# Kernel tuning notes

Hardware: AMD Instinct MI355X
Metric: run time of the kernel (lower is better)

## Reference

```python
import jax, jax.numpy as jnp
import numpy as np

NUM_HEADS = 12
NUM_LANDMARKS = 64


def iterative_inv(K, n_iter=6):
    # K: [B, H, L, L]; Newton-Schulz-style pseudo-inverse iteration
    I = jnp.eye(K.shape[-1], dtype=K.dtype)
    denom = jnp.max(jnp.sum(K, axis=-2), axis=-1)[..., None, None]  # [B,H,1,1]
    V = jnp.swapaxes(K, -1, -2) / denom
    for _ in range(n_iter):
        KV = K @ V
        V = 0.25 * V @ (13.0 * I - KV @ (15.0 * I - KV @ (7.0 * I - KV)))
    return V


def setup_inputs() -> dict:
    key = jax.random.key(0)
    k1, k2, k3, k4 = jax.random.split(key, 4)
    B, N, C = 8, 4096, 768
    x = jax.random.normal(k1, (B, N, C), dtype=jnp.float32)
    w_qkv = jax.random.normal(k2, (C, 3 * C), dtype=jnp.float32) * 0.02
    w_proj = jax.random.normal(k3, (C, C), dtype=jnp.float32) * 0.02
    b_proj = jax.random.normal(k4, (C,), dtype=jnp.float32) * 0.02
    return {"x": x, "w_qkv": w_qkv, "w_proj": w_proj, "b_proj": b_proj}


def reference(x, w_qkv, w_proj, b_proj):
    B, N, C = x.shape
    H, L = NUM_HEADS, NUM_LANDMARKS
    D = C // H
    scale = D ** 0.5

    qkv = (x @ w_qkv).reshape(B, N, 3, H, D)
    qkv = jnp.transpose(qkv, (2, 0, 3, 1, 4))  # [3, B, H, N, D]
    Q, K, V = qkv[0] / scale, qkv[1], qkv[2]

    segs = N // L  # r == 0 path (N divisible by L)
    K_lm = K.reshape(B, H, L, segs, D).mean(axis=-2)  # [B,H,L,D]
    Q_lm = Q.reshape(B, H, L, segs, D).mean(axis=-2)

    kernel1 = jax.nn.softmax(jnp.einsum('bhnd,bhld->bhnl', Q, K_lm), axis=-1)   # [B,H,N,L]
    kernel2 = jax.nn.softmax(jnp.einsum('bhld,bhmd->bhlm', Q_lm, K_lm), axis=-1)  # [B,H,L,L]
    kernel3 = jax.nn.softmax(jnp.einsum('bhld,bhnd->bhln', Q_lm, K), axis=-1)   # [B,H,L,N]

    SV = (kernel1 @ iterative_inv(kernel2)) @ (kernel3 @ V)  # [B,H,N,D]

    SV = jnp.transpose(SV, (0, 2, 1, 3)).reshape(B, N, C)
    out = SV @ w_proj + b_proj
    out = out + jnp.transpose(V, (0, 2, 1, 3)).reshape(B, N, C)
    return out
```

## Files before the change

### kernel.cpp

```cpp
#include <hip/hip_runtime.h>
#include <math.h>

#define BB   8
#define NN   4096
#define CC   768
#define HH   12
#define DD   64
#define LL   64
#define BH   96
#define MM_  32768
#define KQKV 768
#define NQKV 2304
#define NTILES 24

typedef short bf16x8 __attribute__((ext_vector_type(8)));
typedef float f32x4  __attribute__((ext_vector_type(4)));

union U4 { unsigned long long ll; unsigned short s[4]; };

__device__ __forceinline__ unsigned short f2bf(float f) {
  union { float f; unsigned u; } v; v.f = f;
  return (unsigned short)((v.u + 0x7FFFu + ((v.u >> 16) & 1u)) >> 16);
}
__device__ __forceinline__ float bf2f(unsigned short h) {
  union { unsigned u; float f; } v; v.u = ((unsigned)h) << 16;
  return v.f;
}
__device__ __forceinline__ f32x4 fzero4() {
  f32x4 z; z[0] = 0.f; z[1] = 0.f; z[2] = 0.f; z[3] = 0.f; return z;
}
__device__ __forceinline__ void gload_lds16(const void* g, void* l) {
  __builtin_amdgcn_global_load_lds(
      (const __attribute__((address_space(1))) void*)g,
      (__attribute__((address_space(3))) void*)l, 16, 0, 0);
}

__global__ __launch_bounds__(256) void prep(
    const float* __restrict__ x, short* __restrict__ xb,
    const float* __restrict__ w_qkv, short* __restrict__ wqkvT,
    const float* __restrict__ w_proj, short* __restrict__ wprojT) {
  __shared__ float tile[32][33];
  int bid = blockIdx.x;
  if (bid < 24576) {
    int i = bid * 256 + threadIdx.x;
    float4 v = ((const float4*)x)[i];
    U4 p; p.s[0] = f2bf(v.x); p.s[1] = f2bf(v.y); p.s[2] = f2bf(v.z); p.s[3] = f2bf(v.w);
    ((unsigned long long*)xb)[i] = p.ll;
    return;
  }
  const float* in; short* out; int R, C, c0, r0;
  if (bid < 26304) {
    int j = bid - 24576;
    in = w_qkv; out = wqkvT; R = KQKV; C = NQKV;
    c0 = (j % 72) * 32; r0 = (j / 72) * 32;
  } else {
    int j = bid - 26304;
    in = w_proj; out = wprojT; R = CC; C = CC;
    c0 = (j % 24) * 32; r0 = (j / 24) * 32;
  }
  int tx = threadIdx.x & 31, ty = threadIdx.x >> 5;
  for (int i = ty; i < 32; i += 8)
    tile[i][tx] = in[(r0 + i) * C + c0 + tx];
  __syncthreads();
  for (int i = ty; i < 32; i += 8)
    out[(c0 + i) * R + r0 + tx] = (short)f2bf(tile[tx][i]);
}

template <int EPI>
__global__ __launch_bounds__(256, 3) void gemm128(
    const short* __restrict__ A, const short* __restrict__ Bw,
    short* __restrict__ o0, short* __restrict__ o1, short* __restrict__ o2,
    const float* __restrict__ bias, float* __restrict__ fout,
    short* __restrict__ Qlmb, short* __restrict__ Klmb,
    float* __restrict__ QlmF, float* __restrict__ KlmF) {
  __shared__ short L[24576];
  const int t = threadIdx.x;
  const int wave = t >> 6, lane = t & 63;
  const int wr = (wave >> 1) << 6, wc = (wave & 1) << 6;
  const int lrow = lane & 15, g = lane >> 4;

  const int x = (int)blockIdx.x & 7;
  const int local = (int)blockIdx.x >> 3;
  int tm, tn;
  if constexpr (EPI == 0) {
    const int phase = local / 288;
    const int r = local % 288;
    tm = x * 32 + r / 9;
    tn = phase * 9 + r % 9;
  } else {
    tm = x * 32 + local / 6;
    tn = local % 6;
  }
  const int m0 = tm << 7;

  const int csl = (((t & 3) ^ ((t >> 3) & 3)) << 3);
  const short* pA0 = A  + (size_t)(m0 + (t >> 2)) * KQKV + csl;
  const short* pA1 = pA0 + 64 * KQKV;
  const short* pB0 = Bw + (size_t)(tn * 128 + (t >> 2)) * KQKV + csl;
  const short* pB1 = pB0 + 64 * KQKV;
  char* dA = (char*)L + t * 16;
  char* dB = (char*)L + 8192 + t * 16;

  const int swz = ((g ^ ((lrow >> 1) & 3)) << 4);
  const int aoff = (wr + lrow) * 64 + swz;
  const int boff = 8192 + (wc + lrow) * 64 + swz;

  f32x4 acc[4][4];
#pragma unroll
  for (int i = 0; i < 4; ++i)
#pragma unroll
    for (int j = 0; j < 4; ++j) acc[i][j] = fzero4();

#pragma unroll
  for (int T = 0; T < 2; ++T) {
    gload_lds16(pA0 + T * 32, dA + T * 16384);
    gload_lds16(pA1 + T * 32, dA + T * 16384 + 4096);
    gload_lds16(pB0 + T * 32, dB + T * 16384);
    gload_lds16(pB1 + T * 32, dB + T * 16384 + 4096);
  }
  asm volatile("s_waitcnt vmcnt(4)" ::: "memory");
  __builtin_amdgcn_s_barrier();

  for (int T = 0; T < NTILES; ++T) {
    const int Ts = T + 2;
    if (Ts < NTILES) {
      const int sb = (Ts % 3) * 16384;
      gload_lds16(pA0 + Ts * 32, dA + sb);
      gload_lds16(pA1 + Ts * 32, dA + sb + 4096);
      gload_lds16(pB0 + Ts * 32, dB + sb);
      gload_lds16(pB1 + Ts * 32, dB + sb + 4096);
    }
    const char* Lb = (const char*)L + (T % 3) * 16384;
    bf16x8 a[4], b[4];
#pragma unroll
    for (int nf = 0; nf < 4; ++nf) b[nf] = *(const bf16x8*)(Lb + boff + nf * 1024);
#pragma unroll
    for (int rf = 0; rf < 4; ++rf) a[rf] = *(const bf16x8*)(Lb + aoff + rf * 1024);
#pragma unroll
    for (int rf = 0; rf < 4; ++rf)
#pragma unroll
      for (int nf = 0; nf < 4; ++nf)
        acc[rf][nf] = __builtin_amdgcn_mfma_f32_16x16x32_bf16(a[rf], b[nf], acc[rf][nf], 0, 0, 0);
    if (T < NTILES - 2)       { asm volatile("s_waitcnt vmcnt(4)" ::: "memory"); }
    else if (T == NTILES - 2) { asm volatile("s_waitcnt vmcnt(0)" ::: "memory"); }
    __builtin_amdgcn_s_barrier();
  }

  if constexpr (EPI == 0) {
    const int cg0 = tn * 128;
    const int three = cg0 / 768;
    const int ccb = cg0 % 768;
    short* dst = (three == 0) ? o0 : (three == 1) ? o1 : o2;
    const float sc = (three == 0) ? 0.125f : 1.f;
    short* LS = (short*)L;
#pragma unroll
    for (int rf = 0; rf < 4; ++rf)
#pragma unroll
      for (int nf = 0; nf < 4; ++nf)
#pragma unroll
        for (int i = 0; i < 4; ++i)
          LS[(wr + rf * 16 + g * 4 + i) * 144 + wc + nf * 16 + lrow] =
              (short)f2bf(acc[rf][nf][i] * sc);
    __syncthreads();
#pragma unroll
    for (int k = 0; k < 8; ++k) {
      int id = t + k * 256;
      int row = id >> 4, ch = id & 15;
      bf16x8 v = *(const bf16x8*)&LS[row * 144 + ch * 8];
      int c = ccb + ch * 8, h = c >> 6, d = c & 63;
      int r = m0 + row, bb = r >> 12, n = r & 4095;
      *(bf16x8*)&dst[((size_t)(bb * HH + h) * NN + n) * DD + d] = v;
    }
    if (three < 2) {
      int seg = t >> 7, col = t & 127;
      float ssum = 0.f;
#pragma unroll
      for (int j = 0; j < 64; ++j) ssum += bf2f((unsigned short)LS[(seg * 64 + j) * 144 + col]);
      ssum *= (1.f / 64.f);
      int l = ((tm & 31) << 1) + seg;
      int c = ccb + col, h = c >> 6, d = c & 63;
      int bh = (tm >> 5) * HH + h;
      int idx = bh * 4096 + l * 64 + d;
      if (three == 0) { QlmF[idx] = ssum; Qlmb[idx] = (short)f2bf(ssum); }
      else            { KlmF[idx] = ssum; Klmb[idx] = (short)f2bf(ssum); }
    }
  } else {
    float* LF = (float*)L;
#pragma unroll
    for (int pass = 0; pass < 2; ++pass) {
      if ((wave >> 1) == pass) {
#pragma unroll
        for (int rf = 0; rf < 4; ++rf)
#pragma unroll
          for (int nf = 0; nf < 4; ++nf)
#pragma unroll
            for (int i = 0; i < 4; ++i)
              LF[(rf * 16 + g * 4 + i) * 136 + wc + nf * 16 + lrow] = acc[rf][nf][i];
      }
      __syncthreads();
#pragma unroll
      for (int k = 0; k < 8; ++k) {
        int id = t + k * 256;
        int row = id >> 5, ch = id & 31;
        float4 v = *(const float4*)&LF[row * 136 + ch * 4];
        int R = m0 + pass * 64 + row;
        int c = tn * 128 + ch * 4;
        int bb = R >> 12, n = R & 4095, h = c >> 6, d = c & 63;
        float4 bi = *(const float4*)&bias[c];
        U4 r4;
        r4.ll = *(const unsigned long long*)&o2[((size_t)(bb * HH + h) * NN + n) * DD + d];
        v.x += bi.x + bf2f(r4.s[0]);
        v.y += bi.y + bf2f(r4.s[1]);
        v.z += bi.z + bf2f(r4.s[2]);
        v.w += bi.w + bf2f(r4.s[3]);
        *(float4*)&fout[(size_t)R * CC + c] = v;
      }
      __syncthreads();
    }
  }
}

__global__ __launch_bounds__(256) void e12(
    const short* __restrict__ Kb, const short* __restrict__ Vb,
    const short* __restrict__ Qlmb,
    float* __restrict__ k3VTp, float* __restrict__ s3part) {
  int bh = blockIdx.y, chunk = blockIdx.x;
  __shared__ short Qlm[64 * 72];
  __shared__ short Plds[64 * 136];
  __shared__ short Vl[128 * 68];
  int t = threadIdx.x;
  for (int r = 0; r < 2; r++) {
    int e = t + r * 256;
    *(bf16x8*)&Qlm[(e >> 3) * 72 + (e & 7) * 8] = *(const bf16x8*)&Qlmb[bh * 4096 + e * 8];
  }
  int wave = t >> 6, lane = t & 63, lrow = lane & 15, g = lane >> 4, lk = g << 3;
  f32x4 o2[4];
  float cpl[4];
#pragma unroll
  for (int lf = 0; lf < 4; lf++) { o2[lf] = fzero4(); cpl[lf] = 0.f; }
  const int dloc = wave * 16 + lrow;

  for (int s = 0; s < 4; ++s) {
    int nb = chunk * 512 + s * 128;
    __syncthreads();
#pragma unroll
    for (int r = 0; r < 4; r++) {
      int id = t + r * 256;
      int n = id >> 3, c8 = id & 7;
      unsigned long long v1 = *(const unsigned long long*)&Vb[((size_t)bh * NN + nb + n) * DD + c8 * 8];
      unsigned long long v2 = *(const unsigned long long*)&Vb[((size_t)bh * NN + nb + n) * DD + c8 * 8 + 4];
      *(unsigned long long*)&Vl[n * 68 + c8 * 8] = v1;
      *(unsigned long long*)&Vl[n * 68 + c8 * 8 + 4] = v2;
    }
    int nw = nb + wave * 32;
    bf16x8 aK[2][2];
#pragma unroll
    for (int rf = 0; rf < 2; rf++)
#pragma unroll
      for (int ks = 0; ks < 2; ks++)
        aK[rf][ks] = *(const bf16x8*)&Kb[((size_t)bh * NN + nw + rf * 16 + lrow) * DD + ks * 32 + lk];
    f32x4 acc[2][4];
#pragma unroll
    for (int rf = 0; rf < 2; rf++)
#pragma unroll
      for (int lf = 0; lf < 4; lf++) acc[rf][lf] = fzero4();
#pragma unroll
    for (int ks = 0; ks < 2; ks++) {
      bf16x8 bq[4];
#pragma unroll
      for (int lf = 0; lf < 4; lf++)
        bq[lf] = *(const bf16x8*)&Qlm[(lf * 16 + lrow) * 72 + ks * 32 + lk];
#pragma unroll
      for (int rf = 0; rf < 2; rf++)
#pragma unroll
        for (int lf = 0; lf < 4; lf++)
          acc[rf][lf] = __builtin_amdgcn_mfma_f32_16x16x32_bf16(aK[rf][ks], bq[lf], acc[rf][lf], 0, 0, 0);
    }
#pragma unroll
    for (int lf = 0; lf < 4; lf++) {
      int l = lf * 16 + lrow;
#pragma unroll
      for (int rf = 0; rf < 2; rf++) {
        U4 p;
#pragma unroll
        for (int i = 0; i < 4; i++) {
          float e = expf(acc[rf][lf][i]);
          p.s[i] = f2bf(e); cpl[lf] += e;
        }
        *(unsigned long long*)&Plds[l * 136 + wave * 32 + rf * 16 + g * 4] = p.ll;
      }
    }
    __syncthreads();
#pragma unroll
    for (int ks = 0; ks < 4; ++ks) {
      bf16x8 a;
#pragma unroll
      for (int j = 0; j < 8; ++j) a[j] = Vl[(ks * 32 + lk + j) * 68 + dloc];
#pragma unroll
      for (int lf = 0; lf < 4; lf++) {
        bf16x8 b = *(const bf16x8*)&Plds[(lf * 16 + lrow) * 136 + ks * 32 + lk];
        o2[lf] = __builtin_amdgcn_mfma_f32_16x16x32_bf16(a, b, o2[lf], 0, 0, 0);
      }
    }
  }
#pragma unroll
  for (int lf = 0; lf < 4; lf++) {
    float cp = cpl[lf];
    cp += __shfl_xor(cp, 16);
    cp += __shfl_xor(cp, 32);
    if (lane < 16)
      s3part[((bh * 8 + chunk) * 4 + wave) * LL + lf * 16 + lane] = cp;
    int l = lf * 16 + lrow;
#pragma unroll
    for (int i = 0; i < 4; i++) {
      int dd = wave * 16 + g * 4 + i;
      k3VTp[((size_t)chunk * BH + bh) * 4096 + dd * 64 + l] = o2[lf][i];
    }
  }
}

__device__ __forceinline__ void mm64(const float* X, const float* Y, int row, int c0, float o[8]) {
#pragma unroll
  for (int j = 0; j < 8; j++) o[j] = 0.f;
  for (int k = 0; k < 64; k++) {
    float x = X[row * 68 + k];
    const float4* yp = (const float4*)&Y[k * 68 + c0];
    float4 y0 = yp[0], y1 = yp[1];
    o[0] += x * y0.x; o[1] += x * y0.y; o[2] += x * y0.z; o[3] += x * y0.w;
    o[4] += x * y1.x; o[5] += x * y1.y; o[6] += x * y1.z; o[7] += x * y1.w;
  }
}

__global__ __launch_bounds__(512) void newton_inv(
    const float* __restrict__ QlmF, const float* __restrict__ KlmF,
    const float* __restrict__ k3VTp, const float* __restrict__ s3part,
    short* __restrict__ MTws) {
  __shared__ float A_[64 * 68], B_[64 * 68], C_[64 * 68], D_[64 * 68], E_[64 * 68];
  __shared__ float red[64];
  __shared__ float denom_s;
  int bh = blockIdx.x, t = threadIdx.x;
  int row = t >> 3, c0 = (t & 7) << 3;
#pragma unroll
  for (int i = 0; i < 8; i++) {
    int e = t * 8 + i;
    A_[(e >> 6) * 68 + (e & 63)] = QlmF[bh * 4096 + e];
    B_[(e >> 6) * 68 + (e & 63)] = KlmF[bh * 4096 + e];
  }
  __syncthreads();
  {
    float4 ar[16];
#pragma unroll
    for (int q = 0; q < 16; q++) ar[q] = *(const float4*)&A_[row * 68 + q * 4];
    float o[8];
#pragma unroll
    for (int mm = 0; mm < 8; mm++) {
      const float4* br = (const float4*)&B_[(c0 + mm) * 68];
      float s = 0.f;
      for (int q = 0; q < 16; q++) {
        float4 b4 = br[q];
        s += ar[q].x * b4.x + ar[q].y * b4.y + ar[q].z * b4.z + ar[q].w * b4.w;
      }
      o[mm] = s;
    }
    float mx = o[0];
#pragma unroll
    for (int mm = 1; mm < 8; mm++) mx = fmaxf(mx, o[mm]);
    mx = fmaxf(mx, __shfl_xor(mx, 1));
    mx = fmaxf(mx, __shfl_xor(mx, 2));
    mx = fmaxf(mx, __shfl_xor(mx, 4));
    float ss = 0.f;
#pragma unroll
    for (int mm = 0; mm < 8; mm++) { o[mm] = expf(o[mm] - mx); ss += o[mm]; }
    ss += __shfl_xor(ss, 1); ss += __shfl_xor(ss, 2); ss += __shfl_xor(ss, 4);
    float r = 1.f / ss;
#pragma unroll
    for (int mm = 0; mm < 8; mm++) C_[row * 68 + c0 + mm] = o[mm] * r;
  }
  __syncthreads();
  if (t < 64) {
    float s = 0.f;
    for (int l2 = 0; l2 < 64; l2++) s += C_[l2 * 68 + t];
    red[t] = s;
  }
  __syncthreads();
  if (t == 0) {
    float m = red[0];
    for (int i = 1; i < 64; i++) m = fmaxf(m, red[i]);
    denom_s = m;
  }
  __syncthreads();
  {
    float rdn = 1.f / denom_s;
#pragma unroll
    for (int i = 0; i < 8; i++) D_[row * 68 + c0 + i] = C_[(c0 + i) * 68 + row] * rdn;
  }
  __syncthreads();
  float* Vc = D_;
  float* t1 = A_;
  float* t2 = B_;
  float* t3 = E_;
  float o[8];
  for (int it = 0; it < 6; it++) {
    mm64(C_, Vc, row, c0, o);
#pragma unroll
    for (int j = 0; j < 8; j++) t1[row * 68 + c0 + j] = o[j];
    __syncthreads();
    mm64(t1, t1, row, c0, o);
#pragma unroll
    for (int j = 0; j < 8; j++) t2[row * 68 + c0 + j] = 7.f * t1[row * 68 + c0 + j] - o[j];
    __syncthreads();
    mm64(t1, t2, row, c0, o);
#pragma unroll
    for (int j = 0; j < 8; j++) t3[row * 68 + c0 + j] = 15.f * t1[row * 68 + c0 + j] - o[j];
    __syncthreads();
    mm64(Vc, t3, row, c0, o);
#pragma unroll
    for (int j = 0; j < 8; j++) t2[row * 68 + c0 + j] = 0.25f * (13.f * Vc[row * 68 + c0 + j] - o[j]);
    __syncthreads();
    float* tmp = Vc; Vc = t2; t2 = tmp;
  }
  if (t < 64) {
    float s = 0.f;
    for (int i2 = 0; i2 < 32; i2++) s += s3part[(bh * 32 + i2) * LL + t];
    red[t] = 1.f / s;
  }
  __syncthreads();
#pragma unroll
  for (int i = 0; i < 8; i++) {
    int e = t * 8 + i;
    float s = 0.f;
#pragma unroll
    for (int c = 0; c < 8; c++) s += k3VTp[((size_t)c * BH + bh) * 4096 + e];
    t1[(e >> 6) * 68 + (e & 63)] = s * red[e & 63];
  }
  __syncthreads();
  {
    float4 ar[16];
#pragma unroll
    for (int q = 0; q < 16; q++) ar[q] = *(const float4*)&t1[row * 68 + q * 4];
    for (int jj = 0; jj < 8; jj++) {
      const float4* dr = (const float4*)&Vc[(c0 + jj) * 68];
      float s = 0.f;
      for (int q = 0; q < 16; q++) {
        float4 d4 = dr[q];
        s += ar[q].x * d4.x + ar[q].y * d4.y + ar[q].z * d4.z + ar[q].w * d4.w;
      }
      MTws[bh * 4096 + row * 64 + c0 + jj] = (short)f2bf(s);
    }
  }
}

__global__ __launch_bounds__(256) void pass2(
    const short* __restrict__ Qb, const short* __restrict__ Klmb,
    const short* __restrict__ MTws, short* __restrict__ SVb) {
  int bh = blockIdx.y, n0 = blockIdx.x * 128;
  int bb = bh / HH, hh = bh % HH;
  __shared__ short Klm[64 * 72];
  __shared__ short Mt[64 * 72];
  __shared__ short Pl[128 * 72];
  int t = threadIdx.x;
  for (int r = 0; r < 2; r++) {
    int e = t + r * 256;
    *(bf16x8*)&Klm[(e >> 3) * 72 + (e & 7) * 8] = *(const bf16x8*)&Klmb[bh * 4096 + e * 8];
    *(bf16x8*)&Mt[(e >> 3) * 72 + (e & 7) * 8]  = *(const bf16x8*)&MTws[bh * 4096 + e * 8];
  }
  __syncthreads();
  int wave = t >> 6, lane = t & 63, lrow = lane & 15, lk = (lane >> 4) << 3;
  int nw = wave * 32;
  bf16x8 aQ[2][2];
#pragma unroll
  for (int rf = 0; rf < 2; rf++)
#pragma unroll
    for (int ks = 0; ks < 2; ks++)
      aQ[rf][ks] = *(const bf16x8*)&Qb[((size_t)bh * NN + n0 + nw + rf * 16 + lrow) * DD + ks * 32 + lk];
  f32x4 s[2][4];
#pragma unroll
  for (int rf = 0; rf < 2; rf++)
#pragma unroll
    for (int jf = 0; jf < 4; jf++) s[rf][jf] = fzero4();
#pragma unroll
  for (int ks = 0; ks < 2; ks++) {
    bf16x8 bk[4];
#pragma unroll
    for (int jf = 0; jf < 4; jf++)
      bk[jf] = *(const bf16x8*)&Klm[(jf * 16 + lrow) * 72 + ks * 32 + lk];
#pragma unroll
    for (int rf = 0; rf < 2; rf++)
#pragma unroll
      for (int jf = 0; jf < 4; jf++)
        s[rf][jf] = __builtin_amdgcn_mfma_f32_16x16x32_bf16(aQ[rf][ks], bk[jf], s[rf][jf], 0, 0, 0);
  }
#pragma unroll
  for (int rf = 0; rf < 2; rf++)
#pragma unroll
    for (int i = 0; i < 4; i++) {
      float v0 = s[rf][0][i], v1 = s[rf][1][i], v2 = s[rf][2][i], v3 = s[rf][3][i];
      float mx = fmaxf(fmaxf(v0, v1), fmaxf(v2, v3));
      mx = fmaxf(mx, __shfl_xor(mx, 1));
      mx = fmaxf(mx, __shfl_xor(mx, 2));
      mx = fmaxf(mx, __shfl_xor(mx, 4));
      mx = fmaxf(mx, __shfl_xor(mx, 8));
      v0 = expf(v0 - mx); v1 = expf(v1 - mx); v2 = expf(v2 - mx); v3 = expf(v3 - mx);
      float ss = v0 + v1 + v2 + v3;
      ss += __shfl_xor(ss, 1); ss += __shfl_xor(ss, 2);
      ss += __shfl_xor(ss, 4); ss += __shfl_xor(ss, 8);
      float rr = 1.f / ss;
      int n = nw + rf * 16 + ((lane >> 4) << 2) + i;
      Pl[n * 72 + 0  + lrow] = (short)f2bf(v0 * rr);
      Pl[n * 72 + 16 + lrow] = (short)f2bf(v1 * rr);
      Pl[n * 72 + 32 + lrow] = (short)f2bf(v2 * rr);
      Pl[n * 72 + 48 + lrow] = (short)f2bf(v3 * rr);
    }
  __syncthreads();
  f32x4 o[2][4];
#pragma unroll
  for (int rf = 0; rf < 2; rf++)
#pragma unroll
    for (int df = 0; df < 4; df++) o[rf][df] = fzero4();
#pragma unroll
  for (int ks = 0; ks < 2; ks++) {
    bf16x8 aP[2];
#pragma unroll
    for (int rf = 0; rf < 2; rf++)
      aP[rf] = *(const bf16x8*)&Pl[(nw + rf * 16 + lrow) * 72 + ks * 32 + lk];
    bf16x8 bm[4];
#pragma unroll
    for (int df = 0; df < 4; df++)
      bm[df] = *(const bf16x8*)&Mt[(df * 16 + lrow) * 72 + ks * 32 + lk];
#pragma unroll
    for (int rf = 0; rf < 2; rf++)
#pragma unroll
      for (int df = 0; df < 4; df++)
        o[rf][df] = __builtin_amdgcn_mfma_f32_16x16x32_bf16(aP[rf], bm[df], o[rf][df], 0, 0, 0);
  }
#pragma unroll
  for (int rf = 0; rf < 2; rf++)
#pragma unroll
    for (int df = 0; df < 4; df++)
#pragma unroll
      for (int i = 0; i < 4; i++) {
        int n = n0 + nw + rf * 16 + ((lane >> 4) << 2) + i;
        SVb[((size_t)bb * NN + n) * CC + hh * 64 + df * 16 + lrow] = (short)f2bf(o[rf][df][i]);
      }
}

extern "C" void kernel_launch(void* const* d_in, const int* in_sizes, int n_in,
                              void* d_out, int out_size, void* d_ws, size_t ws_size,
                              hipStream_t stream) {
  const float* x      = (const float*)d_in[0];
  const float* w_qkv  = (const float*)d_in[1];
  const float* w_proj = (const float*)d_in[2];
  const float* b_proj = (const float*)d_in[3];
  float* out = (float*)d_out;

  char* p = (char*)d_ws;
  auto alloc = [&](size_t bytes) -> char* {
    char* r = p; p += (bytes + 255) & ~(size_t)255; return r;
  };
  short* xb     = (short*)alloc((size_t)MM_ * KQKV * 2);
  short* wqkvT  = (short*)alloc((size_t)NQKV * KQKV * 2);
  short* wprojT = (short*)alloc((size_t)CC * CC * 2);
  short* Qb     = (short*)alloc((size_t)BH * NN * DD * 2);
  short* Kb     = (short*)alloc((size_t)BH * NN * DD * 2);
  short* Vb     = (short*)alloc((size_t)BH * NN * DD * 2);
  short* Qlmb   = (short*)alloc((size_t)BH * LL * DD * 2);
  short* Klmb   = (short*)alloc((size_t)BH * LL * DD * 2);
  float* QlmF   = (float*)alloc((size_t)BH * LL * DD * 4);
  float* KlmF   = (float*)alloc((size_t)BH * LL * DD * 4);
  float* s3part = (float*)alloc((size_t)BH * 32 * LL * 4);
  float* k3VTp  = (float*)alloc((size_t)8 * BH * DD * LL * 4);
  short* MTws   = (short*)alloc((size_t)BH * DD * LL * 2);
  short* SVb    = (short*)alloc((size_t)MM_ * CC * 2);

  prep<<<26880, 256, 0, stream>>>(x, xb, w_qkv, wqkvT, w_proj, wprojT);
  gemm128<0><<<dim3((MM_ / 128) * (NQKV / 128)), 256, 0, stream>>>(
      xb, wqkvT, Qb, Kb, Vb, nullptr, nullptr, Qlmb, Klmb, QlmF, KlmF);
  e12<<<dim3(8, BH), 256, 0, stream>>>(Kb, Vb, Qlmb, k3VTp, s3part);
  newton_inv<<<BH, 512, 0, stream>>>(QlmF, KlmF, k3VTp, s3part, MTws);
  pass2<<<dim3(NN / 128, BH), 256, 0, stream>>>(Qb, Klmb, MTws, SVb);
  gemm128<1><<<dim3((MM_ / 128) * (CC / 128)), 256, 0, stream>>>(
      SVb, wprojT, nullptr, nullptr, Vb, b_proj, out,
      nullptr, nullptr, nullptr, nullptr);
}
```

Measured before the change: 376.1 us.

## Run Newton-Schulz inverse matmuls on MFMA with split-bf16 precision

Replaces the scalar fp32 shared-memory 64x64 matmuls in the iterative inverse with bf16 MFMA instructions. Each operand is split into high and low bf16 parts, and three MFMAs per product approximate fp32 accuracy. Operands are kept in both row-major and column-major shared buffers. The goal is to cut the ALU-bound cost of the small per-head inversion kernel, at the price of extra conversion work and more barriers. It also risks some precision loss in the iteration.

```diff
diff --git a/kernel.cpp b/kernel.cpp
--- a/kernel.cpp
+++ b/kernel.cpp
@@ -319,27 +319,28 @@
   }
 }
 
-__device__ __forceinline__ void mm64(const float* X, const float* Y, int row, int c0, float o[8]) {
-#pragma unroll
-  for (int j = 0; j < 8; j++) o[j] = 0.f;
-  for (int k = 0; k < 64; k++) {
-    float x = X[row * 68 + k];
-    const float4* yp = (const float4*)&Y[k * 68 + c0];
-    float4 y0 = yp[0], y1 = yp[1];
-    o[0] += x * y0.x; o[1] += x * y0.y; o[2] += x * y0.z; o[3] += x * y0.w;
-    o[4] += x * y1.x; o[5] += x * y1.y; o[6] += x * y1.z; o[7] += x * y1.w;
-  }
-}
-
 __global__ __launch_bounds__(512) void newton_inv(
     const float* __restrict__ QlmF, const float* __restrict__ KlmF,
     const float* __restrict__ k3VTp, const float* __restrict__ s3part,
     short* __restrict__ MTws) {
-  __shared__ float A_[64 * 68], B_[64 * 68], C_[64 * 68], D_[64 * 68], E_[64 * 68];
+  __shared__ float Cf[64 * 68];
+  __shared__ short BUF[12 * 4608];
   __shared__ float red[64];
   __shared__ float denom_s;
-  int bh = blockIdx.x, t = threadIdx.x;
-  int row = t >> 3, c0 = (t & 7) << 3;
+  short* Crm_h  = BUF + 0 * 4608;  short* Crm_l  = BUF + 1 * 4608;
+  short* Vrm_h  = BUF + 2 * 4608;  short* Vrm_l  = BUF + 3 * 4608;
+  short* Vcm_h  = BUF + 4 * 4608;  short* Vcm_l  = BUF + 5 * 4608;
+  short* T1rm_h = BUF + 6 * 4608;  short* T1rm_l = BUF + 7 * 4608;
+  short* T1cm_h = BUF + 8 * 4608;  short* T1cm_l = BUF + 9 * 4608;
+  short* T2cm_h = BUF + 10 * 4608; short* T2cm_l = BUF + 11 * 4608;
+  float* A_ = (float*)BUF;
+  float* B_ = A_ + 64 * 68;
+
+  const int bh = blockIdx.x, t = threadIdx.x;
+  const int row = t >> 3, c0 = (t & 7) << 3;
+  const int wv = t >> 6, lane = t & 63, lrow = lane & 15, g = lane >> 4;
+  const int rw = (wv >> 1) * 16, cw = (wv & 1) * 32;
+
 #pragma unroll
   for (int i = 0; i < 8; i++) {
     int e = t * 8 + i;
@@ -374,12 +375,12 @@
     ss += __shfl_xor(ss, 1); ss += __shfl_xor(ss, 2); ss += __shfl_xor(ss, 4);
     float r = 1.f / ss;
 #pragma unroll
-    for (int mm = 0; mm < 8; mm++) C_[row * 68 + c0 + mm] = o[mm] * r;
+    for (int mm = 0; mm < 8; mm++) Cf[row * 68 + c0 + mm] = o[mm] * r;
   }
   __syncthreads();
   if (t < 64) {
     float s = 0.f;
-    for (int l2 = 0; l2 < 64; l2++) s += C_[l2 * 68 + t];
+    for (int l2 = 0; l2 < 64; l2++) s += Cf[l2 * 68 + t];
     red[t] = s;
   }
   __syncthreads();
@@ -392,33 +393,110 @@
   {
     float rdn = 1.f / denom_s;
 #pragma unroll
-    for (int i = 0; i < 8; i++) D_[row * 68 + c0 + i] = C_[(c0 + i) * 68 + row] * rdn;
-  }
-  __syncthreads();
-  float* Vc = D_;
-  float* t1 = A_;
-  float* t2 = B_;
-  float* t3 = E_;
-  float o[8];
-  for (int it = 0; it < 6; it++) {
-    mm64(C_, Vc, row, c0, o);
-#pragma unroll
-    for (int j = 0; j < 8; j++) t1[row * 68 + c0 + j] = o[j];
-    __syncthreads();
-    mm64(t1, t1, row, c0, o);
-#pragma unroll
-    for (int j = 0; j < 8; j++) t2[row * 68 + c0 + j] = 7.f * t1[row * 68 + c0 + j] - o[j];
-    __syncthreads();
-    mm64(t1, t2, row, c0, o);
-#pragma unroll
-    for (int j = 0; j < 8; j++) t3[row * 68 + c0 + j] = 15.f * t1[row * 68 + c0 + j] - o[j];
-    __syncthreads();
-    mm64(Vc, t3, row, c0, o);
-#pragma unroll
-    for (int j = 0; j < 8; j++) t2[row * 68 + c0 + j] = 0.25f * (13.f * Vc[row * 68 + c0 + j] - o[j]);
-    __syncthreads();
-    float* tmp = Vc; Vc = t2; t2 = tmp;
-  }
+    for (int i = 0; i < 8; i++) {
+      int e = t * 8 + i, r = e >> 6, c = e & 63;
+      float cv = Cf[r * 68 + c];
+      unsigned short chh = f2bf(cv);
+      Crm_h[r * 72 + c] = (short)chh;
+      Crm_l[r * 72 + c] = (short)f2bf(cv - bf2f(chh));
+      float vv = Cf[c * 68 + r] * rdn;
+      unsigned short vh = f2bf(vv);
+      unsigned short vl = f2bf(vv - bf2f(vh));
+      Vrm_h[r * 72 + c] = (short)vh; Vrm_l[r * 72 + c] = (short)vl;
+      Vcm_h[c * 72 + r] = (short)vh; Vcm_l[c * 72 + r] = (short)vl;
+    }
+  }
+  __syncthreads();
+
+  f32x4 acc[2];
+  auto mfmm = [&](const short* Xh, const short* Xl, const short* Yh, const short* Yl) {
+    acc[0] = fzero4(); acc[1] = fzero4();
+#pragma unroll
+    for (int ks = 0; ks < 2; ++ks) {
+      bf16x8 ah = *(const bf16x8*)&Xh[(rw + lrow) * 72 + ks * 32 + g * 8];
+      bf16x8 al = *(const bf16x8*)&Xl[(rw + lrow) * 72 + ks * 32 + g * 8];
+#pragma unroll
+      for (int cf = 0; cf < 2; ++cf) {
+        const int c = cw + cf * 16 + lrow;
+        bf16x8 bhv = *(const bf16x8*)&Yh[c * 72 + ks * 32 + g * 8];
+        bf16x8 blv = *(const bf16x8*)&Yl[c * 72 + ks * 32 + g * 8];
+        acc[cf] = __builtin_amdgcn_mfma_f32_16x16x32_bf16(ah, bhv, acc[cf], 0, 0, 0);
+        acc[cf] = __builtin_amdgcn_mfma_f32_16x16x32_bf16(ah, blv, acc[cf], 0, 0, 0);
+        acc[cf] = __builtin_amdgcn_mfma_f32_16x16x32_bf16(al, bhv, acc[cf], 0, 0, 0);
+      }
+    }
+  };
+  auto storeRM = [&](short* H, short* Lo) {
+#pragma unroll
+    for (int cf = 0; cf < 2; ++cf)
+#pragma unroll
+      for (int i = 0; i < 4; ++i) {
+        float z = acc[cf][i];
+        unsigned short h = f2bf(z);
+        int r = rw + g * 4 + i, c = cw + cf * 16 + lrow;
+        H[r * 72 + c] = (short)h;
+        Lo[r * 72 + c] = (short)f2bf(z - bf2f(h));
+      }
+  };
+  auto storeCM = [&](short* H, short* Lo) {
+#pragma unroll
+    for (int cf = 0; cf < 2; ++cf) {
+      U4 ph, pl;
+#pragma unroll
+      for (int i = 0; i < 4; ++i) {
+        float z = acc[cf][i];
+        unsigned short h = f2bf(z);
+        ph.s[i] = h; pl.s[i] = f2bf(z - bf2f(h));
+      }
+      int c = cw + cf * 16 + lrow;
+      *(unsigned long long*)&H[c * 72 + rw + g * 4] = ph.ll;
+      *(unsigned long long*)&Lo[c * 72 + rw + g * 4] = pl.ll;
+    }
+  };
+
+  float t1v[2][4];
+  for (int it = 0; it < 6; ++it) {
+    mfmm(Crm_h, Crm_l, Vcm_h, Vcm_l);
+    __syncthreads();
+    storeRM(T1rm_h, T1rm_l); storeCM(T1cm_h, T1cm_l);
+    __syncthreads();
+    mfmm(T1rm_h, T1rm_l, T1cm_h, T1cm_l);
+#pragma unroll
+    for (int cf = 0; cf < 2; ++cf)
+#pragma unroll
+      for (int i = 0; i < 4; ++i) {
+        int r = rw + g * 4 + i, c = cw + cf * 16 + lrow;
+        t1v[cf][i] = bf2f((unsigned short)T1rm_h[r * 72 + c]) +
+                     bf2f((unsigned short)T1rm_l[r * 72 + c]);
+        acc[cf][i] = 7.f * t1v[cf][i] - acc[cf][i];
+      }
+    __syncthreads();
+    storeCM(T2cm_h, T2cm_l);
+    __syncthreads();
+    mfmm(T1rm_h, T1rm_l, T2cm_h, T2cm_l);
+#pragma unroll
+    for (int cf = 0; cf < 2; ++cf)
+#pragma unroll
+      for (int i = 0; i < 4; ++i)
+        acc[cf][i] = 15.f * t1v[cf][i] - acc[cf][i];
+    __syncthreads();
+    storeCM(T2cm_h, T2cm_l);
+    __syncthreads();
+    mfmm(Vrm_h, Vrm_l, T2cm_h, T2cm_l);
+#pragma unroll
+    for (int cf = 0; cf < 2; ++cf)
+#pragma unroll
+      for (int i = 0; i < 4; ++i) {
+        int r = rw + g * 4 + i, c = cw + cf * 16 + lrow;
+        float v0 = bf2f((unsigned short)Vrm_h[r * 72 + c]) +
+                   bf2f((unsigned short)Vrm_l[r * 72 + c]);
+        acc[cf][i] = 0.25f * (13.f * v0 - acc[cf][i]);
+      }
+    __syncthreads();
+    storeRM(Vrm_h, Vrm_l); storeCM(Vcm_h, Vcm_l);
+    __syncthreads();
+  }
+
   if (t < 64) {
     float s = 0.f;
     for (int i2 = 0; i2 < 32; i2++) s += s3part[(bh * 32 + i2) * LL + t];
@@ -427,27 +505,23 @@
   __syncthreads();
 #pragma unroll
   for (int i = 0; i < 8; i++) {
-    int e = t * 8 + i;
+    int e = t * 8 + i, d = e >> 6, m = e & 63;
     float s = 0.f;
 #pragma unroll
     for (int c = 0; c < 8; c++) s += k3VTp[((size_t)c * BH + bh) * 4096 + e];
-    t1[(e >> 6) * 68 + (e & 63)] = s * red[e & 63];
-  }
-  __syncthreads();
-  {
-    float4 ar[16];
-#pragma unroll
-    for (int q = 0; q < 16; q++) ar[q] = *(const float4*)&t1[row * 68 + q * 4];
-    for (int jj = 0; jj < 8; jj++) {
-      const float4* dr = (const float4*)&Vc[(c0 + jj) * 68];
-      float s = 0.f;
-      for (int q = 0; q < 16; q++) {
-        float4 d4 = dr[q];
-        s += ar[q].x * d4.x + ar[q].y * d4.y + ar[q].z * d4.z + ar[q].w * d4.w;
-      }
-      MTws[bh * 4096 + row * 64 + c0 + jj] = (short)f2bf(s);
-    }
-  }
+    s *= red[m];
+    unsigned short h = f2bf(s);
+    T1rm_h[d * 72 + m] = (short)h;
+    T1rm_l[d * 72 + m] = (short)f2bf(s - bf2f(h));
+  }
+  __syncthreads();
+  mfmm(T1rm_h, T1rm_l, Vrm_h, Vrm_l);
+#pragma unroll
+  for (int cf = 0; cf < 2; ++cf)
+#pragma unroll
+    for (int i = 0; i < 4; ++i)
+      MTws[bh * 4096 + (rw + g * 4 + i) * 64 + cw + cf * 16 + lrow] =
+          (short)f2bf(acc[cf][i]);
 }
 
 __global__ __launch_bounds__(256) void pass2(
```

Result: faster. 334.2 us, median of 2 (-11.1%).
